# Optimization experiments

Measured on AMD Instinct MI355X. Metric: run time of the kernel, lower is better.

## Reference

```python
import jax, jax.numpy as jnp
import numpy as np

ACT_BITS = 8  # global_act_bit in the original repo
QMAX = float(2 ** ACT_BITS - 1)


def _fake_quant_asym(x):
    """Asymmetric per-tensor fake quantization (weight_quant_fn, activate=True)."""
    mx = jnp.max(x)
    mn = jnp.min(x)
    scale = (mx - mn) / QMAX
    zp = jnp.round(-mn / scale)
    q = jnp.clip(jnp.round(x / scale) + zp, 0.0, QMAX)
    return (q - zp) * scale


def setup_inputs() -> dict:
    key = jax.random.key(0)
    kx, kq, kr, kl, ks = jax.random.split(key, 5)
    B, S, IN, OUT, R = 32, 1024, 1152, 1152, 64
    x = jax.random.normal(kx, (B, S, IN), dtype=jnp.float32)
    quant_w = jax.random.normal(kq, (OUT, IN), dtype=jnp.float32) * 0.02  # quant.weight
    right_w = jax.random.normal(kr, (R, IN), dtype=jnp.float32) * 0.02   # right.weight
    left_w = jax.random.normal(kl, (OUT, R), dtype=jnp.float32) * 0.02   # left.weight
    bias = jnp.zeros((OUT,), dtype=jnp.float32)
    scales = jax.random.uniform(ks, (IN,), dtype=jnp.float32, minval=0.5, maxval=2.0)
    return {"x": x, "quant_w": quant_w, "right_w": right_w,
            "left_w": left_w, "bias": bias, "scales": scales}


def reference(x, quant_w, right_w, left_w, bias, scales):
    # inference path, merge=False: smooth-quant style scale division, then
    # asymmetric per-tensor fake quant, then quant GEMM + low-rank SVD adapter.
    xs = x / scales                                   # [B,S,IN] elementwise
    xq = _fake_quant_asym(xs)                         # global max/min fake quant
    hx = jnp.einsum('bsi,oi->bso', xq, quant_w)       # quantized linear
    lrx = jnp.einsum('bsr,or->bso',
                     jnp.einsum('bsi,ri->bsr', xq, right_w), left_w)  # low-rank
    return hx + lrx + bias
```

## Files before the change

### kernel.cpp

```cpp
#include <hip/hip_runtime.h>
#include <hip/hip_bf16.h>
#include <stdint.h>

#define M_DIM   32768
#define IN_DIM  1152
#define OUT_DIM 1152
#define R_DIM   64
#define QMAXF   255.0f

#define RED_BLOCKS 4096
#define QBLOCKS    4096

typedef float  f32x4  __attribute__((ext_vector_type(4)));
typedef __bf16 bf16x8 __attribute__((ext_vector_type(8)));

static __device__ __forceinline__ unsigned short f2bf(float f) {
    unsigned int u = __float_as_uint(f);
    unsigned int r = (u + 0x7fffu + ((u >> 16) & 1u)) >> 16;
    return (unsigned short)r;
}

__global__ __launch_bounds__(256) void k_minmax(const float* __restrict__ x,
                                                const float* __restrict__ scales,
                                                float* __restrict__ partials) {
    const int n4 = (M_DIM * IN_DIM) / 4;
    int tid = blockIdx.x * 256 + threadIdx.x;
    const int stride = RED_BLOCKS * 256;
    float mn = 3.4e38f, mx = -3.4e38f;
    for (int i4 = tid; i4 < n4; i4 += stride) {
        int i = i4 * 4;
        float4 xv = *(const float4*)(x + i);
        int c = i % IN_DIM;
        float4 sv = *(const float4*)(scales + c);
        float a0 = xv.x / sv.x, a1 = xv.y / sv.y;
        float a2 = xv.z / sv.z, a3 = xv.w / sv.w;
        mn = fminf(mn, fminf(fminf(a0, a1), fminf(a2, a3)));
        mx = fmaxf(mx, fmaxf(fmaxf(a0, a1), fmaxf(a2, a3)));
    }
    #pragma unroll
    for (int off = 32; off > 0; off >>= 1) {
        mn = fminf(mn, __shfl_down(mn, off));
        mx = fmaxf(mx, __shfl_down(mx, off));
    }
    __shared__ float smn[4], smx[4];
    int lane = threadIdx.x & 63, wv = threadIdx.x >> 6;
    if (lane == 0) { smn[wv] = mn; smx[wv] = mx; }
    __syncthreads();
    if (threadIdx.x == 0) {
        float bmn = fminf(fminf(smn[0], smn[1]), fminf(smn[2], smn[3]));
        float bmx = fmaxf(fmaxf(smx[0], smx[1]), fmaxf(smx[2], smx[3]));
        partials[blockIdx.x * 2]     = bmn;
        partials[blockIdx.x * 2 + 1] = bmx;
    }
}

__global__ __launch_bounds__(256) void k_finalize(const float* __restrict__ partials,
                                                  float* __restrict__ qp) {
    float mn = 3.4e38f, mx = -3.4e38f;
    for (int i = threadIdx.x; i < RED_BLOCKS; i += 256) {
        mn = fminf(mn, partials[i * 2]);
        mx = fmaxf(mx, partials[i * 2 + 1]);
    }
    #pragma unroll
    for (int off = 32; off > 0; off >>= 1) {
        mn = fminf(mn, __shfl_down(mn, off));
        mx = fmaxf(mx, __shfl_down(mx, off));
    }
    __shared__ float smn[4], smx[4];
    int lane = threadIdx.x & 63, wv = threadIdx.x >> 6;
    if (lane == 0) { smn[wv] = mn; smx[wv] = mx; }
    __syncthreads();
    if (threadIdx.x == 0) {
        float bmn = fminf(fminf(smn[0], smn[1]), fminf(smn[2], smn[3]));
        float bmx = fmaxf(fmaxf(smx[0], smx[1]), fmaxf(smx[2], smx[3]));
        float qs = (bmx - bmn) / QMAXF;
        float zp = rintf(-bmn / qs);
        qp[0] = qs;
        qp[1] = zp;
    }
}

__global__ __launch_bounds__(256) void k_quant(const float* __restrict__ x,
                                               const float* __restrict__ scales,
                                               const float* __restrict__ qp,
                                               unsigned short* __restrict__ xq) {
    const float qs = qp[0], zp = qp[1];
    const int n4 = (M_DIM * IN_DIM) / 4;
    int tid = blockIdx.x * 256 + threadIdx.x;
    const int stride = QBLOCKS * 256;
    for (int i4 = tid; i4 < n4; i4 += stride) {
        int i = i4 * 4;
        float4 xv = *(const float4*)(x + i);
        int c = i % IN_DIM;
        float4 sv = *(const float4*)(scales + c);
        float a[4] = { xv.x / sv.x, xv.y / sv.y, xv.z / sv.z, xv.w / sv.w };
        ushort4 o;
        unsigned short* op = (unsigned short*)&o;
        #pragma unroll
        for (int j = 0; j < 4; j++) {
            float q = rintf(a[j] / qs) + zp;
            q = fminf(fmaxf(q, 0.0f), QMAXF);
            op[j] = f2bf(q - zp);
        }
        *(ushort4*)(xq + i) = o;
    }
}

__global__ __launch_bounds__(256) void k_wprep(const float* __restrict__ qw,
                                               const float* __restrict__ rw,
                                               const float* __restrict__ lw,
                                               unsigned short* __restrict__ wc) {
    int idx = blockIdx.x * 256 + threadIdx.x;
    int o = idx / IN_DIM;
    int i = idx - o * IN_DIM;
    float acc = qw[idx];
    #pragma unroll 8
    for (int r = 0; r < R_DIM; r++)
        acc += lw[o * R_DIM + r] * rw[r * IN_DIM + i];
    wc[idx] = f2bf(acc);
}

#define BM 128
#define BN 128
#define BK 32

__global__ __launch_bounds__(256) void k_gemm(const unsigned short* __restrict__ A,
                                              const unsigned short* __restrict__ Bw,
                                              const float* __restrict__ bias,
                                              const float* __restrict__ qp,
                                              float* __restrict__ C) {
    __shared__ __align__(16) unsigned short As[BM * BK];
    __shared__ __align__(16) unsigned short Bs[BN * BK];
    const int tid = threadIdx.x;
    const int bm = blockIdx.x, bn = blockIdx.y;
    const int K = IN_DIM, N = OUT_DIM;

    const int r0 = tid >> 2;
    const int c0 = (tid & 3) * 8;
    const unsigned short* ga0 = A  + (size_t)(bm * BM + r0) * K + c0;
    const unsigned short* ga1 = ga0 + (size_t)64 * K;
    const unsigned short* gb0 = Bw + (size_t)(bn * BN + r0) * K + c0;
    const unsigned short* gb1 = gb0 + (size_t)64 * K;
    unsigned short* lA0 = As + tid * 8;
    unsigned short* lA1 = As + tid * 8 + 2048;
    unsigned short* lB0 = Bs + tid * 8;
    unsigned short* lB1 = Bs + tid * 8 + 2048;

    f32x4 acc[4][4];
    #pragma unroll
    for (int mi = 0; mi < 4; mi++)
        #pragma unroll
        for (int ni = 0; ni < 4; ni++)
            acc[mi][ni] = (f32x4)0.0f;

    const int lane = tid & 63, wv = tid >> 6;
    const int wm = (wv & 1) * 64;
    const int wn = (wv >> 1) * 64;
    const int l16 = lane & 15, l4 = lane >> 4;
    const bf16x8* Asv = (const bf16x8*)As;
    const bf16x8* Bsv = (const bf16x8*)Bs;
    const int afo = (wm + l16) * 4 + l4;
    const int bfo = (wn + l16) * 4 + l4;

    for (int k0 = 0; k0 < K; k0 += BK) {
        __builtin_amdgcn_global_load_lds(
            (const __attribute__((address_space(1))) unsigned int*)(ga0 + k0),
            (__attribute__((address_space(3))) unsigned int*)lA0, 16, 0, 0);
        __builtin_amdgcn_global_load_lds(
            (const __attribute__((address_space(1))) unsigned int*)(ga1 + k0),
            (__attribute__((address_space(3))) unsigned int*)lA1, 16, 0, 0);
        __builtin_amdgcn_global_load_lds(
            (const __attribute__((address_space(1))) unsigned int*)(gb0 + k0),
            (__attribute__((address_space(3))) unsigned int*)lB0, 16, 0, 0);
        __builtin_amdgcn_global_load_lds(
            (const __attribute__((address_space(1))) unsigned int*)(gb1 + k0),
            (__attribute__((address_space(3))) unsigned int*)lB1, 16, 0, 0);
        __syncthreads();

        bf16x8 af[4], bf[4];
        #pragma unroll
        for (int mi = 0; mi < 4; mi++) af[mi] = Asv[afo + mi * 64];
        #pragma unroll
        for (int ni = 0; ni < 4; ni++) bf[ni] = Bsv[bfo + ni * 64];
        #pragma unroll
        for (int mi = 0; mi < 4; mi++)
            #pragma unroll
            for (int ni = 0; ni < 4; ni++)
                acc[mi][ni] = __builtin_amdgcn_mfma_f32_16x16x32_bf16(
                    af[mi], bf[ni], acc[mi][ni], 0, 0, 0);
        __syncthreads();
    }

    const float qs = qp[0];
    #pragma unroll
    for (int mi = 0; mi < 4; mi++) {
        int row0 = bm * BM + wm + mi * 16 + l4 * 4;
        #pragma unroll
        for (int ni = 0; ni < 4; ni++) {
            int col = bn * BN + wn + ni * 16 + l16;
            float bv = bias[col];
            #pragma unroll
            for (int r = 0; r < 4; r++)
                C[(size_t)(row0 + r) * N + col] = acc[mi][ni][r] * qs + bv;
        }
    }
}

extern "C" void kernel_launch(void* const* d_in, const int* in_sizes, int n_in,
                              void* d_out, int out_size, void* d_ws, size_t ws_size,
                              hipStream_t stream) {
    const float* x      = (const float*)d_in[0];
    const float* qw     = (const float*)d_in[1];
    const float* rw     = (const float*)d_in[2];
    const float* lw     = (const float*)d_in[3];
    const float* bias   = (const float*)d_in[4];
    const float* scales = (const float*)d_in[5];

    char* ws = (char*)d_ws;
    unsigned short* xq = (unsigned short*)ws;
    unsigned short* wc = (unsigned short*)(ws + 75497472);
    float* partials    = (float*)(ws + 75497472 + 2654208);
    float* qp          = (float*)(ws + 75497472 + 2654208 + 32768);

    k_minmax  <<<RED_BLOCKS, 256, 0, stream>>>(x, scales, partials);
    k_finalize<<<1,          256, 0, stream>>>(partials, qp);
    k_quant   <<<QBLOCKS,    256, 0, stream>>>(x, scales, qp, xq);
    k_wprep   <<<(OUT_DIM * IN_DIM) / 256, 256, 0, stream>>>(qw, rw, lw, wc);

    dim3 grid(M_DIM / BM, OUT_DIM / BN);
    k_gemm<<<grid, 256, 0, stream>>>(xq, wc, bias, qp, (float*)d_out);
}
```

Baseline: 428.9 us.

## Precompute reciprocal scales, simplify quant math, remap GEMM blocks per XCD

```diff
diff --git a/kernel.cpp b/kernel.cpp
--- a/kernel.cpp
+++ b/kernel.cpp
@@ -8,7 +8,7 @@
 #define R_DIM   64
 #define QMAXF   255.0f
 
-#define RED_BLOCKS 4096
+#define RED_BLOCKS 2048
 #define QBLOCKS    4096
 
 typedef float  f32x4  __attribute__((ext_vector_type(4)));
@@ -20,8 +20,25 @@
     return (unsigned short)r;
 }
 
+__global__ __launch_bounds__(256) void k_wprep(const float* __restrict__ qw,
+                                               const float* __restrict__ rw,
+                                               const float* __restrict__ lw,
+                                               const float* __restrict__ scales,
+                                               unsigned short* __restrict__ wc,
+                                               float* __restrict__ rs) {
+    int idx = blockIdx.x * 256 + threadIdx.x;
+    if (idx < IN_DIM) rs[idx] = 1.0f / scales[idx];
+    int o = idx / IN_DIM;
+    int i = idx - o * IN_DIM;
+    float acc = qw[idx];
+    #pragma unroll 8
+    for (int r = 0; r < R_DIM; r++)
+        acc += lw[o * R_DIM + r] * rw[r * IN_DIM + i];
+    wc[idx] = f2bf(acc);
+}
+
 __global__ __launch_bounds__(256) void k_minmax(const float* __restrict__ x,
-                                                const float* __restrict__ scales,
+                                                const float* __restrict__ rs,
                                                 float* __restrict__ partials) {
     const int n4 = (M_DIM * IN_DIM) / 4;
     int tid = blockIdx.x * 256 + threadIdx.x;
@@ -31,9 +48,9 @@
         int i = i4 * 4;
         float4 xv = *(const float4*)(x + i);
         int c = i % IN_DIM;
-        float4 sv = *(const float4*)(scales + c);
-        float a0 = xv.x / sv.x, a1 = xv.y / sv.y;
-        float a2 = xv.z / sv.z, a3 = xv.w / sv.w;
+        float4 sv = *(const float4*)(rs + c);
+        float a0 = xv.x * sv.x, a1 = xv.y * sv.y;
+        float a2 = xv.z * sv.z, a3 = xv.w * sv.w;
         mn = fminf(mn, fminf(fminf(a0, a1), fminf(a2, a3)));
         mx = fmaxf(mx, fmaxf(fmaxf(a0, a1), fmaxf(a2, a3)));
     }
@@ -55,7 +72,9 @@
 }
 
 __global__ __launch_bounds__(256) void k_finalize(const float* __restrict__ partials,
-                                                  float* __restrict__ qp) {
+                                                  const float* __restrict__ scales,
+                                                  float* __restrict__ qp,
+                                                  float* __restrict__ comb) {
     float mn = 3.4e38f, mx = -3.4e38f;
     for (int i = threadIdx.x; i < RED_BLOCKS; i += 256) {
         mn = fminf(mn, partials[i * 2]);
@@ -67,6 +86,7 @@
         mx = fmaxf(mx, __shfl_down(mx, off));
     }
     __shared__ float smn[4], smx[4];
+    __shared__ float s_qs;
     int lane = threadIdx.x & 63, wv = threadIdx.x >> 6;
     if (lane == 0) { smn[wv] = mn; smx[wv] = mx; }
     __syncthreads();
@@ -77,14 +97,21 @@
         float zp = rintf(-bmn / qs);
         qp[0] = qs;
         qp[1] = zp;
-    }
+        qp[2] = -zp;
+        qp[3] = QMAXF - zp;
+        s_qs = qs;
+    }
+    __syncthreads();
+    float qs = s_qs;
+    for (int c = threadIdx.x; c < IN_DIM; c += 256)
+        comb[c] = 1.0f / (scales[c] * qs);
 }
 
 __global__ __launch_bounds__(256) void k_quant(const float* __restrict__ x,
-                                               const float* __restrict__ scales,
+                                               const float* __restrict__ comb,
                                                const float* __restrict__ qp,
                                                unsigned short* __restrict__ xq) {
-    const float qs = qp[0], zp = qp[1];
+    const float lo = qp[2], hi = qp[3];
     const int n4 = (M_DIM * IN_DIM) / 4;
     int tid = blockIdx.x * 256 + threadIdx.x;
     const int stride = QBLOCKS * 256;
@@ -92,32 +119,18 @@
         int i = i4 * 4;
         float4 xv = *(const float4*)(x + i);
         int c = i % IN_DIM;
-        float4 sv = *(const float4*)(scales + c);
-        float a[4] = { xv.x / sv.x, xv.y / sv.y, xv.z / sv.z, xv.w / sv.w };
+        float4 cb = *(const float4*)(comb + c);
+        float a[4] = { xv.x * cb.x, xv.y * cb.y, xv.z * cb.z, xv.w * cb.w };
         ushort4 o;
         unsigned short* op = (unsigned short*)&o;
         #pragma unroll
         for (int j = 0; j < 4; j++) {
-            float q = rintf(a[j] / qs) + zp;
-            q = fminf(fmaxf(q, 0.0f), QMAXF);
-            op[j] = f2bf(q - zp);
+            float q = rintf(a[j]);
+            q = fminf(fmaxf(q, lo), hi);
+            op[j] = f2bf(q);
         }
         *(ushort4*)(xq + i) = o;
     }
-}
-
-__global__ __launch_bounds__(256) void k_wprep(const float* __restrict__ qw,
-                                               const float* __restrict__ rw,
-                                               const float* __restrict__ lw,
-                                               unsigned short* __restrict__ wc) {
-    int idx = blockIdx.x * 256 + threadIdx.x;
-    int o = idx / IN_DIM;
-    int i = idx - o * IN_DIM;
-    float acc = qw[idx];
-    #pragma unroll 8
-    for (int r = 0; r < R_DIM; r++)
-        acc += lw[o * R_DIM + r] * rw[r * IN_DIM + i];
-    wc[idx] = f2bf(acc);
 }
 
 #define BM 128
@@ -132,7 +145,12 @@
     __shared__ __align__(16) unsigned short As[BM * BK];
     __shared__ __align__(16) unsigned short Bs[BN * BK];
     const int tid = threadIdx.x;
-    const int bm = blockIdx.x, bn = blockIdx.y;
+    const int lid = blockIdx.x;
+    const int xcd = lid & 7;
+    const int kk  = lid >> 3;
+    const int bml = kk / 9;
+    const int bn  = kk - bml * 9;
+    const int bm  = xcd * 32 + bml;
     const int K = IN_DIM, N = OUT_DIM;
 
     const int r0 = tid >> 2;
@@ -220,13 +238,14 @@
     unsigned short* xq = (unsigned short*)ws;
     unsigned short* wc = (unsigned short*)(ws + 75497472);
     float* partials    = (float*)(ws + 75497472 + 2654208);
-    float* qp          = (float*)(ws + 75497472 + 2654208 + 32768);
-
-    k_minmax  <<<RED_BLOCKS, 256, 0, stream>>>(x, scales, partials);
-    k_finalize<<<1,          256, 0, stream>>>(partials, qp);
-    k_quant   <<<QBLOCKS,    256, 0, stream>>>(x, scales, qp, xq);
-    k_wprep   <<<(OUT_DIM * IN_DIM) / 256, 256, 0, stream>>>(qw, rw, lw, wc);
-
-    dim3 grid(M_DIM / BM, OUT_DIM / BN);
-    k_gemm<<<grid, 256, 0, stream>>>(xq, wc, bias, qp, (float*)d_out);
-}
+    float* qp          = (float*)(ws + 75497472 + 2654208 + 16384);
+    float* rs          = (float*)(ws + 75497472 + 2654208 + 16384 + 64);
+    float* comb        = (float*)(ws + 75497472 + 2654208 + 16384 + 64 + 4608);
+
+    k_wprep   <<<(OUT_DIM * IN_DIM) / 256, 256, 0, stream>>>(qw, rw, lw, scales, wc, rs);
+    k_minmax  <<<RED_BLOCKS, 256, 0, stream>>>(x, rs, partials);
+    k_finalize<<<1,          256, 0, stream>>>(partials, scales, qp, comb);
+    k_quant   <<<QBLOCKS,    256, 0, stream>>>(x, comb, qp, xq);
+
+    k_gemm<<<2304, 256, 0, stream>>>(xq, wc, bias, qp, (float*)d_out);
+}
```

Measured after the change: 419.3 us. 2.2% less time.
